# Performance work log

Hardware: AMD Instinct MI355X
Metric: run time of the kernel (lower is better)

## Reference

```python
import jax, jax.numpy as jnp
import numpy as np

N = 50000      # nodes
E = 800000     # edges
M = 1000000    # total subgraph membership rows
D = 128        # atom_fea_len
ED = 64        # nbr_fea_len
H = 8          # heads
C = D // H     # per-head dim


def _ln(x, g, b, eps=1e-5):
    mu = x.mean(-1, keepdims=True)
    var = ((x - mu) ** 2).mean(-1, keepdims=True)
    return (x - mu) / jnp.sqrt(var + eps) * g + b


def setup_inputs() -> dict:
    key = jax.random.key(0)
    ks = jax.random.split(key, 16)
    s = 0.05
    inp = {
        "x": jax.random.normal(ks[0], (N, D), jnp.float32),
        "edge_index": jax.random.randint(ks[1], (2, E), 0, N, jnp.int32),
        "edge_attr": jax.random.normal(ks[2], (E, ED), jnp.float32),
        "sub_nodes": jax.random.randint(ks[3], (M,), 0, N, jnp.int32),
        "sub_indicator": jax.random.randint(ks[4], (M,), 0, N, jnp.int32),
        # TransformerConv params (PyG: lin_query/key/value, lin_edge, lin_skip, all with bias)
        "Wq": jax.random.normal(ks[5], (D, D), jnp.float32) * s,
        "bq": jnp.zeros((D,), jnp.float32),
        "Wk": jax.random.normal(ks[6], (D, D), jnp.float32) * s,
        "bk": jnp.zeros((D,), jnp.float32),
        "Wv": jax.random.normal(ks[7], (D, D), jnp.float32) * s,
        "bv": jnp.zeros((D,), jnp.float32),
        "We": jax.random.normal(ks[8], (ED, D), jnp.float32) * s,
        "be": jnp.zeros((D,), jnp.float32),
        "Ws": jax.random.normal(ks[9], (D, D), jnp.float32) * s,
        "bs": jnp.zeros((D,), jnp.float32),
        # subgraph_norm
        "sn_g": jnp.ones((D,), jnp.float32),
        "sn_b": jnp.zeros((D,), jnp.float32),
        # subgraph_proj: Linear -> SiLU -> Linear
        "p1_w": jax.random.normal(ks[10], (D, D), jnp.float32) * s,
        "p1_b": jnp.zeros((D,), jnp.float32),
        "p2_w": jax.random.normal(ks[11], (D, D), jnp.float32) * s,
        "p2_b": jnp.zeros((D,), jnp.float32),
        # out_norm
        "on_g": jnp.ones((D,), jnp.float32),
        "on_b": jnp.zeros((D,), jnp.float32),
    }
    return inp


def reference(x, edge_index, edge_attr, sub_nodes, sub_indicator,
              Wq, bq, Wk, bk, Wv, bv, We, be, Ws, bs,
              sn_g, sn_b, p1_w, p1_b, p2_w, p2_b, on_g, on_b):
    n = x.shape[0]
    src, dst = edge_index[0], edge_index[1]  # messages flow src -> dst (PyG source_to_target)

    # ---- TransformerConv ----
    q = (x @ Wq + bq).reshape(n, H, C)
    k = (x @ Wk + bk).reshape(n, H, C)
    v = (x @ Wv + bv).reshape(n, H, C)
    e = (edge_attr @ We + be).reshape(-1, H, C)       # [E,H,C]
    ke = k[src] + e                                    # edge-conditioned keys
    ve = v[src] + e                                    # edge-conditioned values
    alpha = (q[dst] * ke).sum(-1) / jnp.sqrt(jnp.asarray(C, x.dtype))  # [E,H]
    # scatter-softmax over incoming edges of each dst node
    m = jax.ops.segment_max(alpha, dst, num_segments=n)               # [N,H]
    ea = jnp.exp(alpha - m[dst])
    denom = jax.ops.segment_sum(ea, dst, num_segments=n)              # [N,H]
    num = jax.ops.segment_sum(ea[:, :, None] * ve, dst, num_segments=n)  # [N,H,C]
    attn = num / jnp.where(denom > 0, denom, 1.0)[:, :, None]
    x_trans = attn.reshape(n, H * C) + (x @ Ws + bs)   # concat heads + root skip

    # ---- subgraph branch: gather -> LayerNorm -> MLP -> scatter-mean ----
    sx = x[sub_nodes]                                  # [M,D]
    sx = _ln(sx, sn_g, sn_b)
    sx = jax.nn.silu(sx @ p1_w + p1_b) @ p2_w + p2_b
    cnt = jax.ops.segment_sum(jnp.ones((sx.shape[0],), x.dtype), sub_indicator, num_segments=n)
    sub_x = jax.ops.segment_sum(sx, sub_indicator, num_segments=n) / jnp.maximum(cnt, 1.0)[:, None]

    # ---- combine (dropout is identity in eval) ----
    out = _ln(x + x_trans + sub_x, on_g, on_b)
    return jax.nn.silu(out)
```

## Files before the change

### kernel.cpp

```cpp
#include <hip/hip_runtime.h>
#include <math.h>

#define DD 128
#define EDD 64

typedef __attribute__((ext_vector_type(8))) short bf16x8;
typedef __attribute__((ext_vector_type(4))) float f32x4;

__device__ inline unsigned short f2bf(float f) {
    unsigned int u = __float_as_uint(f);
    u += 0x7FFFu + ((u >> 16) & 1u);
    return (unsigned short)(u >> 16);
}
__device__ inline unsigned int pack2bf16(float lo, float hi) {
    return (unsigned int)f2bf(lo) | ((unsigned int)f2bf(hi) << 16);
}
__device__ inline float bflo(unsigned int u) { return __uint_as_float(u << 16); }
__device__ inline float bfhi(unsigned int u) { return __uint_as_float(u & 0xffff0000u); }

__global__ __launch_bounds__(256) void packw6_kernel(
    const float* __restrict__ w0, const float* __restrict__ w1, const float* __restrict__ w2,
    const float* __restrict__ w3, const float* __restrict__ w4, const float* __restrict__ w5,
    unsigned short* __restrict__ packed)
{
    int which = blockIdx.y;
    const float* w = which == 0 ? w0 : which == 1 ? w1 : which == 2 ? w2
                   : which == 3 ? w3 : which == 4 ? w4 : w5;
    unsigned short* pk = packed + (size_t)which * DD * DD;
    int idx = blockIdx.x * 256 + threadIdx.x;
    if (idx >= DD * DD) return;
    int j    = idx & 7;
    int lane = (idx >> 3) & 63;
    int kt   = (idx >> 9) & 3;
    int ncf  = idx >> 11;
    int kk  = kt * 32 + (lane >> 4) * 8 + j;
    int col = ncf * 16 + (lane & 15);
    pk[idx] = f2bf(w[kk * DD + col]);
}

__device__ inline void gemm_b(const bf16x8 af[4][2], const unsigned short* __restrict__ packB,
                              int wc, int lane, f32x4 acc[2][4])
{
    #pragma unroll
    for (int i = 0; i < 2; i++)
        #pragma unroll
        for (int j = 0; j < 4; j++) acc[i][j] = (f32x4){0.f, 0.f, 0.f, 0.f};
    #pragma unroll
    for (int kt = 0; kt < 4; kt++) {
        #pragma unroll
        for (int nc = 0; nc < 4; nc++) {
            bf16x8 b = *(const bf16x8*)&packB[(((wc * 4 + nc) * 4 + kt) * 64 + lane) * 8];
            acc[0][nc] = __builtin_amdgcn_mfma_f32_16x16x32_bf16(af[kt][0], b, acc[0][nc], 0, 0, 0);
            acc[1][nc] = __builtin_amdgcn_mfma_f32_16x16x32_bf16(af[kt][1], b, acc[1][nc], 0, 0, 0);
        }
    }
}

__global__ __launch_bounds__(256, 4) void lin4_mfma_kernel(
    const float* __restrict__ x,
    const unsigned short* __restrict__ packBq, const float* __restrict__ bq,
    const unsigned short* __restrict__ packBk, const float* __restrict__ bk,
    const unsigned short* __restrict__ packBv, const float* __restrict__ bv,
    const unsigned short* __restrict__ packBs, const float* __restrict__ bs,
    const float* __restrict__ sn_g, const float* __restrict__ sn_b,
    float* __restrict__ q, unsigned short* __restrict__ kplane, unsigned short* __restrict__ vplane,
    float* __restrict__ pre, unsigned int* __restrict__ lnx, int N)
{
    __shared__ unsigned short sxs[64 * DD];
    int tid = threadIdx.x;
    int lane = tid & 63, wid = tid >> 6;
    size_t m0 = (size_t)blockIdx.x * 64;

    {
        float g0 = sn_g[2 * lane], g1 = sn_g[2 * lane + 1];
        float b0 = sn_b[2 * lane], b1 = sn_b[2 * lane + 1];
        #pragma unroll
        for (int r = 0; r < 16; r++) {
            int tr = wid * 16 + r;
            size_t row = m0 + tr;
            float v0 = 0.f, v1 = 0.f;
            if (row < (size_t)N) {
                float2 xv = *(const float2*)&x[row * DD + 2 * lane];
                v0 = xv.x; v1 = xv.y;
            }
            unsigned int uidx = ((unsigned)(tr * 64 + lane)) ^ (((unsigned)tr & 7u) << 2);
            ((unsigned int*)sxs)[uidx] = pack2bf16(v0, v1);
            float s1 = v0 + v1, s2 = v0 * v0 + v1 * v1;
            #pragma unroll
            for (int o = 32; o >= 1; o >>= 1) { s1 += __shfl_xor(s1, o); s2 += __shfl_xor(s2, o); }
            float mean = s1 * (1.f / DD);
            float var  = s2 * (1.f / DD) - mean * mean;
            float rs = rsqrtf(var + 1e-5f);
            if (row < (size_t)N)
                lnx[row * 64 + lane] = pack2bf16((v0 - mean) * rs * g0 + b0,
                                                 (v1 - mean) * rs * g1 + b1);
        }
    }
    __syncthreads();

    int wr = wid >> 1, wc = wid & 1;
    int rA = wr * 32 + (lane & 15);
    int kb = (lane >> 4) * 8;

    bf16x8 af[4][2];
    #pragma unroll
    for (int kt = 0; kt < 4; kt++) {
        int k0 = kt * 32 + kb;
        af[kt][0] = *(const bf16x8*)&sxs[((rA)      * DD + k0) ^ ((rA & 7) << 3)];
        int rA1 = rA + 16;
        af[kt][1] = *(const bf16x8*)&sxs[((rA1)     * DD + k0) ^ ((rA1 & 7) << 3)];
    }

    f32x4 acc[2][4];
    int colb = wc * 64 + (lane & 15);
    int jrow = (lane >> 4) * 4;

    gemm_b(af, packBq, wc, lane, acc);
    #pragma unroll
    for (int mrf = 0; mrf < 2; mrf++) {
        int rbase = wr * 32 + mrf * 16 + jrow;
        #pragma unroll
        for (int nc = 0; nc < 4; nc++) {
            int col = colb + nc * 16;
            float bias = bq[col];
            #pragma unroll
            for (int j = 0; j < 4; j++) {
                size_t row = m0 + rbase + j;
                if (row < (size_t)N) q[row * DD + col] = acc[mrf][nc][j] + bias;
            }
        }
    }
    gemm_b(af, packBk, wc, lane, acc);
    #pragma unroll
    for (int mrf = 0; mrf < 2; mrf++) {
        int rbase = wr * 32 + mrf * 16 + jrow;
        #pragma unroll
        for (int nc = 0; nc < 4; nc++) {
            int col = colb + nc * 16;
            float bias = bk[col];
            #pragma unroll
            for (int j = 0; j < 4; j++) {
                size_t row = m0 + rbase + j;
                if (row < (size_t)N) kplane[row * DD + col] = f2bf(acc[mrf][nc][j] + bias);
            }
        }
    }
    gemm_b(af, packBv, wc, lane, acc);
    #pragma unroll
    for (int mrf = 0; mrf < 2; mrf++) {
        int rbase = wr * 32 + mrf * 16 + jrow;
        #pragma unroll
        for (int nc = 0; nc < 4; nc++) {
            int col = colb + nc * 16;
            float bias = bv[col];
            #pragma unroll
            for (int j = 0; j < 4; j++) {
                size_t row = m0 + rbase + j;
                if (row < (size_t)N) vplane[row * DD + col] = f2bf(acc[mrf][nc][j] + bias);
            }
        }
    }
    gemm_b(af, packBs, wc, lane, acc);
    #pragma unroll
    for (int mrf = 0; mrf < 2; mrf++) {
        int rbase = wr * 32 + mrf * 16 + jrow;
        #pragma unroll
        for (int nc = 0; nc < 4; nc++) {
            int col = colb + nc * 16;
            float bias = bs[col];
            #pragma unroll
            for (int j = 0; j < 4; j++) {
                size_t row = m0 + rbase + j;
                if (row < (size_t)N)
                    pre[row * DD + col] = x[row * DD + col] + acc[mrf][nc][j] + bias;
            }
        }
    }
}

__global__ __launch_bounds__(256, 4) void mlpnode_kernel(
    const unsigned int* __restrict__ lnx,
    const unsigned short* __restrict__ packB1, const float* __restrict__ p1b,
    const unsigned short* __restrict__ packB2, const float* __restrict__ p2b,
    unsigned short* __restrict__ fnode, int N)
{
    __shared__ unsigned short sxs[64 * DD];
    int tid = threadIdx.x;
    int lane = tid & 63, wid = tid >> 6;
    size_t m0 = (size_t)blockIdx.x * 64;

    #pragma unroll
    for (int r = 0; r < 16; r++) {
        int tr = wid * 16 + r;
        size_t row = m0 + tr;
        unsigned int val = (row < (size_t)N) ? lnx[row * 64 + lane] : 0u;
        unsigned int uidx = ((unsigned)(tr * 64 + lane)) ^ (((unsigned)tr & 7u) << 2);
        ((unsigned int*)sxs)[uidx] = val;
    }
    __syncthreads();

    int wr = wid >> 1, wc = wid & 1;
    int rA = wr * 32 + (lane & 15);
    int kb = (lane >> 4) * 8;

    f32x4 acc[2][4];
    #pragma unroll
    for (int i = 0; i < 2; i++)
        #pragma unroll
        for (int j = 0; j < 4; j++) acc[i][j] = (f32x4){0.f, 0.f, 0.f, 0.f};
    #pragma unroll
    for (int kt = 0; kt < 4; kt++) {
        int k0 = kt * 32 + kb;
        bf16x8 a0 = *(const bf16x8*)&sxs[((rA)  * DD + k0) ^ ((rA & 7) << 3)];
        int rA1 = rA + 16;
        bf16x8 a1 = *(const bf16x8*)&sxs[((rA1) * DD + k0) ^ ((rA1 & 7) << 3)];
        #pragma unroll
        for (int nc = 0; nc < 4; nc++) {
            bf16x8 b = *(const bf16x8*)&packB1[(((wc * 4 + nc) * 4 + kt) * 64 + lane) * 8];
            acc[0][nc] = __builtin_amdgcn_mfma_f32_16x16x32_bf16(a0, b, acc[0][nc], 0, 0, 0);
            acc[1][nc] = __builtin_amdgcn_mfma_f32_16x16x32_bf16(a1, b, acc[1][nc], 0, 0, 0);
        }
    }
    __syncthreads();

    {
        float bias1[4];
        #pragma unroll
        for (int nc = 0; nc < 4; nc++) bias1[nc] = p1b[wc * 64 + nc * 16 + (lane & 15)];
        #pragma unroll
        for (int mrf = 0; mrf < 2; mrf++) {
            int rbase = wr * 32 + mrf * 16 + (lane >> 4) * 4;
            #pragma unroll
            for (int nc = 0; nc < 4; nc++) {
                int col = wc * 64 + nc * 16 + (lane & 15);
                #pragma unroll
                for (int j = 0; j < 4; j++) {
                    float h = acc[mrf][nc][j] + bias1[nc];
                    h = h / (1.f + __expf(-h));
                    int rr = rbase + j;
                    sxs[(rr * DD + col) ^ ((rr & 7) << 3)] = f2bf(h);
                }
            }
        }
    }
    __syncthreads();

    f32x4 acc2[2][4];
    #pragma unroll
    for (int i = 0; i < 2; i++)
        #pragma unroll
        for (int j = 0; j < 4; j++) acc2[i][j] = (f32x4){0.f, 0.f, 0.f, 0.f};
    #pragma unroll
    for (int kt = 0; kt < 4; kt++) {
        int k0 = kt * 32 + kb;
        bf16x8 a0 = *(const bf16x8*)&sxs[((rA)  * DD + k0) ^ ((rA & 7) << 3)];
        int rA1 = rA + 16;
        bf16x8 a1 = *(const bf16x8*)&sxs[((rA1) * DD + k0) ^ ((rA1 & 7) << 3)];
        #pragma unroll
        for (int nc = 0; nc < 4; nc++) {
            bf16x8 b = *(const bf16x8*)&packB2[(((wc * 4 + nc) * 4 + kt) * 64 + lane) * 8];
            acc2[0][nc] = __builtin_amdgcn_mfma_f32_16x16x32_bf16(a0, b, acc2[0][nc], 0, 0, 0);
            acc2[1][nc] = __builtin_amdgcn_mfma_f32_16x16x32_bf16(a1, b, acc2[1][nc], 0, 0, 0);
        }
    }

    {
        float bias2[4];
        #pragma unroll
        for (int nc = 0; nc < 4; nc++) bias2[nc] = p2b[wc * 64 + nc * 16 + (lane & 15)];
        #pragma unroll
        for (int mrf = 0; mrf < 2; mrf++) {
            int rbase = wr * 32 + mrf * 16 + (lane >> 4) * 4;
            #pragma unroll
            for (int nc = 0; nc < 4; nc++) {
                int col = wc * 64 + nc * 16 + (lane & 15);
                #pragma unroll
                for (int j = 0; j < 4; j++) {
                    size_t row = m0 + rbase + j;
                    if (row < (size_t)N)
                        fnode[row * DD + col] = f2bf(acc2[mrf][nc][j] + bias2[nc]);
                }
            }
        }
    }
}

__global__ void count2_kernel(const int* __restrict__ dstA, int E,
                              const int* __restrict__ sub_ind, int M,
                              int* __restrict__ deg, int* __restrict__ cnt)
{
    int i = blockIdx.x * blockDim.x + threadIdx.x;
    int stride = gridDim.x * blockDim.x;
    int total = E > M ? E : M;
    for (; i < total; i += stride) {
        if (i < E) atomicAdd(&deg[dstA[i]], 1);
        if (i < M) atomicAdd(&cnt[sub_ind[i]], 1);
    }
}

__global__ __launch_bounds__(1024) void bscan_kernel(
    const int* __restrict__ inA, const int* __restrict__ inB,
    int* __restrict__ exA, int* __restrict__ exB,
    int* __restrict__ bsA, int* __restrict__ bsB, int N)
{
    const int* in = blockIdx.y ? inB : inA;
    int* ex = blockIdx.y ? exB : exA;
    int* bs = blockIdx.y ? bsB : bsA;
    __shared__ int s[1024];
    int tid = threadIdx.x;
    int i = blockIdx.x * 1024 + tid;
    int val = (i < N) ? in[i] : 0;
    s[tid] = val; __syncthreads();
    for (int off = 1; off < 1024; off <<= 1) {
        int t = (tid >= off) ? s[tid - off] : 0;
        __syncthreads();
        s[tid] += t;
        __syncthreads();
    }
    if (i < N) ex[i] = s[tid] - val;
    if (tid == 1023) bs[blockIdx.x] = s[1023];
}

__global__ void bsum_kernel(int* __restrict__ bsA, int* __restrict__ bsB,
                            int* __restrict__ indptrA, int* __restrict__ indptrB,
                            int nb, int N)
{
    int which = threadIdx.x;
    if (which < 2) {
        int* bs = which ? bsB : bsA;
        int* indptr = which ? indptrB : indptrA;
        int run = 0;
        for (int b = 0; b < nb; b++) { int v = bs[b]; bs[b] = run; run += v; }
        indptr[N] = run;
    }
}

__global__ void bfix_kernel(int* __restrict__ exA, int* __restrict__ fillA, const int* __restrict__ bsA,
                            int* __restrict__ exB, int* __restrict__ fillB, const int* __restrict__ bsB,
                            int N)
{
    int i = blockIdx.x * blockDim.x + threadIdx.x;
    if (i < N) {
        int vA = exA[i] + bsA[i >> 10];
        exA[i] = vA; fillA[i] = vA;
        int vB = exB[i] + bsB[i >> 10];
        exB[i] = vB; fillB[i] = vB;
    }
}

__global__ void escatter_kernel(const int* __restrict__ srcA, const int* __restrict__ dstA, int E,
                                int* __restrict__ fill, int2* __restrict__ spair)
{
    int i = blockIdx.x * blockDim.x + threadIdx.x;
    int stride = gridDim.x * blockDim.x;
    for (; i < E; i += stride) {
        int d = dstA[i];
        int pos = atomicAdd(&fill[d], 1);
        spair[pos] = make_int2(srcA[i], i);
    }
}

__global__ void sscatter_kernel(const int* __restrict__ sub_nodes, const int* __restrict__ sub_ind,
                                int M, int* __restrict__ sfill, int* __restrict__ snode)
{
    int i = blockIdx.x * blockDim.x + threadIdx.x;
    int stride = gridDim.x * blockDim.x;
    for (; i < M; i += stride) {
        int seg = sub_ind[i];
        int pos = atomicAdd(&sfill[seg], 1);
        snode[pos] = sub_nodes[i];
    }
}

__global__ __launch_bounds__(256) void qprep_kernel(
    const float* __restrict__ q, const float* __restrict__ We,
    unsigned int* __restrict__ qweU, int N)
{
    int tid = threadIdx.x;
    int wave = tid >> 6, lane = tid & 63;
    int n = blockIdx.x * 4 + wave;
    if (n >= N) return;
    int jj = lane & 7, g = lane >> 3;
    int hc0 = g * 16;
    const float4* qp = (const float4*)&q[(size_t)n * DD + hc0];
    float4 q0 = qp[0], q1 = qp[1], q2 = qp[2], q3 = qp[3];
    float qWe[8];
    #pragma unroll
    for (int r = 0; r < 8; r++) {
        const float4* wp = (const float4*)&We[(size_t)(8 * jj + r) * DD + hc0];
        float4 wa = wp[0], wb = wp[1], wc = wp[2], wd = wp[3];
        qWe[r] = q0.x * wa.x + q0.y * wa.y + q0.z * wa.z + q0.w * wa.w
               + q1.x * wb.x + q1.y * wb.y + q1.z * wb.z + q1.w * wb.w
               + q2.x * wc.x + q2.y * wc.y + q2.z * wc.z + q2.w * wc.w
               + q3.x * wd.x + q3.y * wd.y + q3.z * wd.z + q3.w * wd.w;
    }
    uint4 packed;
    packed.x = pack2bf16(qWe[0], qWe[1]);
    packed.y = pack2bf16(qWe[2], qWe[3]);
    packed.z = pack2bf16(qWe[4], qWe[5]);
    packed.w = pack2bf16(qWe[6], qWe[7]);
    *(uint4*)&qweU[(size_t)n * 256 + 4 * lane] = packed;
}

__global__ __launch_bounds__(256, 5) void attn_kernel(
    const float* __restrict__ q,
    const unsigned int* __restrict__ kplane32, const unsigned int* __restrict__ vplane32,
    const float* __restrict__ edge_attr, const unsigned int* __restrict__ qweU,
    const float* __restrict__ We, const float* __restrict__ be,
    const int* __restrict__ indptr, const int2* __restrict__ spair,
    float* __restrict__ pre, int N)
{
    int tid = threadIdx.x;
    int wave = tid >> 6, lane = tid & 63;
    int n = blockIdx.x * 4 + wave;
    if (n >= N) return;

    int gbase = lane & 56;
    int jj = lane & 7;
    int c0 = lane * 2;

    float2 qv  = *(const float2*)&q[(size_t)n * DD + c0];
    float2 bev = *(const float2*)&be[c0];

    float t = qv.x * bev.x + qv.y * bev.y;
    t += __shfl_xor(t, 1); t += __shfl_xor(t, 2); t += __shfl_xor(t, 4);
    float qbe4 = t * 0.25f;

    uint4 qw = *(const uint4*)&qweU[(size_t)n * 256 + 4 * lane];
    float qwe0 = bflo(qw.x), qwe1 = bfhi(qw.x), qwe2 = bflo(qw.y), qwe3 = bfhi(qw.y);
    float qwe4 = bflo(qw.z), qwe5 = bfhi(qw.z), qwe6 = bflo(qw.w), qwe7 = bfhi(qw.w);

    int start = indptr[n], end = indptr[n + 1];
    float s = 0.f, av0 = 0.f, av1 = 0.f;
    float aea[8];
    #pragma unroll
    for (int r = 0; r < 8; r++) aea[r] = 0.f;

    int ii = start;
    for (; ii + 3 < end; ii += 4) {
        int2 se[4];
        #pragma unroll
        for (int u = 0; u < 4; u++) se[u] = spair[ii + u];
        float4 ea0[4], ea1[4];
        unsigned int ku[4], vu[4];
        #pragma unroll
        for (int u = 0; u < 4; u++) {
            const float4* eap = (const float4*)&edge_attr[(size_t)se[u].y * EDD + 8 * jj];
            ea0[u] = eap[0];
            ea1[u] = eap[1];
            ku[u] = kplane32[(size_t)se[u].x * 64 + lane];
            vu[u] = vplane32[(size_t)se[u].x * 64 + lane];
        }
        float p[4];
        #pragma unroll
        for (int u = 0; u < 4; u++) {
            float part = qv.x * bflo(ku[u]) + qv.y * bfhi(ku[u])
                       + ea0[u].x * qwe0 + ea0[u].y * qwe1 + ea0[u].z * qwe2 + ea0[u].w * qwe3
                       + ea1[u].x * qwe4 + ea1[u].y * qwe5 + ea1[u].z * qwe6 + ea1[u].w * qwe7;
            part += __shfl_xor(part, 1);
            part += __shfl_xor(part, 2);
            part += __shfl_xor(part, 4);
            p[u] = __expf(part * 0.25f + qbe4);
        }
        #pragma unroll
        for (int u = 0; u < 4; u++) {
            s += p[u];
            av0 += p[u] * bflo(vu[u]);
            av1 += p[u] * bfhi(vu[u]);
            aea[0] += p[u] * ea0[u].x; aea[1] += p[u] * ea0[u].y;
            aea[2] += p[u] * ea0[u].z; aea[3] += p[u] * ea0[u].w;
            aea[4] += p[u] * ea1[u].x; aea[5] += p[u] * ea1[u].y;
            aea[6] += p[u] * ea1[u].z; aea[7] += p[u] * ea1[u].w;
        }
    }
    for (; ii < end; ii++) {
        int2 se = spair[ii];
        const float4* eap = (const float4*)&edge_attr[(size_t)se.y * EDD + 8 * jj];
        float4 ea0 = eap[0];
        float4 ea1 = eap[1];
        unsigned int ku = kplane32[(size_t)se.x * 64 + lane];
        unsigned int vu = vplane32[(size_t)se.x * 64 + lane];
        float part = qv.x * bflo(ku) + qv.y * bfhi(ku)
                   + ea0.x * qwe0 + ea0.y * qwe1 + ea0.z * qwe2 + ea0.w * qwe3
                   + ea1.x * qwe4 + ea1.y * qwe5 + ea1.z * qwe6 + ea1.w * qwe7;
        part += __shfl_xor(part, 1);
        part += __shfl_xor(part, 2);
        part += __shfl_xor(part, 4);
        float p = __expf(part * 0.25f + qbe4);
        s += p;
        av0 += p * bflo(vu);
        av1 += p * bfhi(vu);
        aea[0] += p * ea0.x; aea[1] += p * ea0.y; aea[2] += p * ea0.z; aea[3] += p * ea0.w;
        aea[4] += p * ea1.x; aea[5] += p * ea1.y; aea[6] += p * ea1.z; aea[7] += p * ea1.w;
    }

    if (end > start) {
        float inv = 1.f / s;
        float oe0 = 0.f, oe1 = 0.f;
        #pragma unroll
        for (int m = 0; m < 8; m++) {
            #pragma unroll
            for (int r = 0; r < 8; r++) {
                float a = __shfl(aea[r], gbase + m);
                float2 w = *(const float2*)&We[(size_t)(8 * m + r) * DD + c0];
                oe0 += a * w.x;
                oe1 += a * w.y;
            }
        }
        size_t o = (size_t)n * DD + c0;
        pre[o]     += (av0 + oe0) * inv + bev.x;
        pre[o + 1] += (av1 + oe1) * inv + bev.y;
    }
}

__global__ __launch_bounds__(256) void final2_kernel(
    const float* __restrict__ pre, const unsigned int* __restrict__ fnodeU,
    const int* __restrict__ sindptr, const int* __restrict__ snode,
    const float* __restrict__ on_g, const float* __restrict__ on_b,
    float* __restrict__ out, int N)
{
    int tid = threadIdx.x;
    int wave = tid >> 6, lane = tid & 63;
    int n = blockIdx.x * 4 + wave;
    if (n >= N) return;
    int c0 = 2 * lane;

    int start = sindptr[n], end = sindptr[n + 1];
    float sum0 = 0.f, sum1 = 0.f;
    int ii = start;
    for (; ii + 3 < end; ii += 4) {
        int n0 = snode[ii], n1 = snode[ii + 1], n2 = snode[ii + 2], n3 = snode[ii + 3];
        unsigned int u0 = fnodeU[(size_t)n0 * 64 + lane];
        unsigned int u1 = fnodeU[(size_t)n1 * 64 + lane];
        unsigned int u2 = fnodeU[(size_t)n2 * 64 + lane];
        unsigned int u3 = fnodeU[(size_t)n3 * 64 + lane];
        sum0 += bflo(u0) + bflo(u1) + bflo(u2) + bflo(u3);
        sum1 += bfhi(u0) + bfhi(u1) + bfhi(u2) + bfhi(u3);
    }
    for (; ii < end; ii++) {
        unsigned int u = fnodeU[(size_t)snode[ii] * 64 + lane];
        sum0 += bflo(u);
        sum1 += bfhi(u);
    }
    float inv = 1.f / fmaxf((float)(end - start), 1.f);

    float2 pv = *(const float2*)&pre[(size_t)n * DD + c0];
    float v0 = pv.x + sum0 * inv;
    float v1 = pv.y + sum1 * inv;

    float s1 = v0 + v1, s2 = v0 * v0 + v1 * v1;
    #pragma unroll
    for (int off = 32; off >= 1; off >>= 1) { s1 += __shfl_xor(s1, off); s2 += __shfl_xor(s2, off); }
    float mean = s1 * (1.f / DD);
    float var  = s2 * (1.f / DD) - mean * mean;
    float rs = rsqrtf(var + 1e-5f);

    float2 gv = *(const float2*)&on_g[c0];
    float2 bv = *(const float2*)&on_b[c0];
    float ov0 = (v0 - mean) * rs * gv.x + bv.x;
    float ov1 = (v1 - mean) * rs * gv.y + bv.y;
    float2 res;
    res.x = ov0 / (1.f + __expf(-ov0));
    res.y = ov1 / (1.f + __expf(-ov1));
    *(float2*)&out[(size_t)n * DD + c0] = res;
}

extern "C" void kernel_launch(void* const* d_in, const int* in_sizes, int n_in,
                              void* d_out, int out_size, void* d_ws, size_t ws_size,
                              hipStream_t stream)
{
    const float* x         = (const float*)d_in[0];
    const int*   edge_index= (const int*)  d_in[1];
    const float* edge_attr = (const float*)d_in[2];
    const int*   sub_nodes = (const int*)  d_in[3];
    const int*   sub_ind   = (const int*)  d_in[4];
    const float* Wq = (const float*)d_in[5];  const float* bq = (const float*)d_in[6];
    const float* Wk = (const float*)d_in[7];  const float* bk = (const float*)d_in[8];
    const float* Wv = (const float*)d_in[9];  const float* bv = (const float*)d_in[10];
    const float* We = (const float*)d_in[11]; const float* be = (const float*)d_in[12];
    const float* Ws = (const float*)d_in[13]; const float* bs = (const float*)d_in[14];
    const float* sn_g = (const float*)d_in[15]; const float* sn_b = (const float*)d_in[16];
    const float* p1w = (const float*)d_in[17]; const float* p1b = (const float*)d_in[18];
    const float* p2w = (const float*)d_in[19]; const float* p2b = (const float*)d_in[20];
    const float* on_g = (const float*)d_in[21]; const float* on_b = (const float*)d_in[22];

    int N = in_sizes[0] / DD;
    int E = in_sizes[1] / 2;
    int M = in_sizes[3];
    float* out = (float*)d_out;

    unsigned short* packAll = (unsigned short*)d_ws;
    unsigned short* packB1 = packAll;
    unsigned short* packB2 = packB1 + DD * DD;
    unsigned short* packBq = packB2 + DD * DD;
    unsigned short* packBk = packBq + DD * DD;
    unsigned short* packBv = packBk + DD * DD;
    unsigned short* packBs = packBv + DD * DD;
    size_t ND = (size_t)N * DD;
    float* q     = (float*)(packBs + DD * DD);
    unsigned short* kplane = (unsigned short*)(q + ND);
    unsigned short* vplane = kplane + ND;
    float* pre   = (float*)(vplane + ND);
    unsigned int* qweU  = (unsigned int*)(pre + ND);
    unsigned int* lnx   = qweU + (size_t)N * 256;
    unsigned int* fnode = lnx + (size_t)N * 64;
    int2* spair  = (int2*)(fnode + (size_t)N * 64);
    int* indptr  = (int*)(spair + E);
    int* fill    = indptr + (N + 1);
    int* deg     = fill + N;
    int* cnt     = deg + N;
    int* sindptr = cnt + N;
    int* sfill   = sindptr + (N + 1);
    int* snode   = sfill + N;
    int* bsA     = snode + M;
    int* bsB     = bsA + 64;

    const int* srcA = edge_index;
    const int* dstA = edge_index + E;

    int nb = (N + 1023) / 1024;

    hipMemsetAsync(deg, 0, (size_t)2 * N * sizeof(int), stream);

    {
        dim3 g(64, 6);
        packw6_kernel<<<g, 256, 0, stream>>>(p1w, p2w, Wq, Wk, Wv, Ws, packAll);
    }

    lin4_mfma_kernel<<<(N + 63) / 64, 256, 0, stream>>>(x, packBq, bq, packBk, bk, packBv, bv,
                                                        packBs, bs, sn_g, sn_b,
                                                        q, kplane, vplane, pre, lnx, N);
    mlpnode_kernel<<<(N + 63) / 64, 256, 0, stream>>>(lnx, packB1, p1b, packB2, p2b,
                                                      (unsigned short*)fnode, N);
    count2_kernel<<<2048, 256, 0, stream>>>(dstA, E, sub_ind, M, deg, cnt);
    {
        dim3 g(nb, 2);
        bscan_kernel<<<g, 1024, 0, stream>>>(deg, cnt, indptr, sindptr, bsA, bsB, N);
    }
    bsum_kernel<<<1, 64, 0, stream>>>(bsA, bsB, indptr, sindptr, nb, N);
    bfix_kernel<<<(N + 255) / 256, 256, 0, stream>>>(indptr, fill, bsA, sindptr, sfill, bsB, N);
    escatter_kernel<<<2048, 256, 0, stream>>>(srcA, dstA, E, fill, spair);
    sscatter_kernel<<<2048, 256, 0, stream>>>(sub_nodes, sub_ind, M, sfill, snode);
    qprep_kernel<<<(N + 3) / 4, 256, 0, stream>>>(q, We, qweU, N);
    attn_kernel<<<(N + 3) / 4, 256, 0, stream>>>(q, (const unsigned int*)kplane,
                                                 (const unsigned int*)vplane, edge_attr, qweU,
                                                 We, be, indptr, spair, pre, N);
    final2_kernel<<<(N + 3) / 4, 256, 0, stream>>>(pre, fnode, sindptr, snode, on_g, on_b, out, N);
}
```

Before: 736.6 us.

## Store q in bf16, fuse edge and subgraph scatters, unroll attention by six

```diff
diff --git a/kernel.cpp b/kernel.cpp
--- a/kernel.cpp
+++ b/kernel.cpp
@@ -63,7 +63,8 @@
     const unsigned short* __restrict__ packBv, const float* __restrict__ bv,
     const unsigned short* __restrict__ packBs, const float* __restrict__ bs,
     const float* __restrict__ sn_g, const float* __restrict__ sn_b,
-    float* __restrict__ q, unsigned short* __restrict__ kplane, unsigned short* __restrict__ vplane,
+    unsigned short* __restrict__ qplane,
+    unsigned short* __restrict__ kplane, unsigned short* __restrict__ vplane,
     float* __restrict__ pre, unsigned int* __restrict__ lnx, int N)
 {
     __shared__ unsigned short sxs[64 * DD];
@@ -126,7 +127,7 @@
             #pragma unroll
             for (int j = 0; j < 4; j++) {
                 size_t row = m0 + rbase + j;
-                if (row < (size_t)N) q[row * DD + col] = acc[mrf][nc][j] + bias;
+                if (row < (size_t)N) qplane[row * DD + col] = f2bf(acc[mrf][nc][j] + bias);
             }
         }
     }
@@ -348,32 +349,30 @@
     }
 }
 
-__global__ void escatter_kernel(const int* __restrict__ srcA, const int* __restrict__ dstA, int E,
-                                int* __restrict__ fill, int2* __restrict__ spair)
+__global__ void scatter2_kernel(const int* __restrict__ srcA, const int* __restrict__ dstA, int E,
+                                int* __restrict__ fill, int2* __restrict__ spair,
+                                const int* __restrict__ sub_nodes, const int* __restrict__ sub_ind,
+                                int M, int* __restrict__ sfill, int* __restrict__ snode)
 {
     int i = blockIdx.x * blockDim.x + threadIdx.x;
     int stride = gridDim.x * blockDim.x;
-    for (; i < E; i += stride) {
-        int d = dstA[i];
-        int pos = atomicAdd(&fill[d], 1);
-        spair[pos] = make_int2(srcA[i], i);
-    }
-}
-
-__global__ void sscatter_kernel(const int* __restrict__ sub_nodes, const int* __restrict__ sub_ind,
-                                int M, int* __restrict__ sfill, int* __restrict__ snode)
-{
-    int i = blockIdx.x * blockDim.x + threadIdx.x;
-    int stride = gridDim.x * blockDim.x;
-    for (; i < M; i += stride) {
-        int seg = sub_ind[i];
-        int pos = atomicAdd(&sfill[seg], 1);
-        snode[pos] = sub_nodes[i];
+    int total = E > M ? E : M;
+    for (; i < total; i += stride) {
+        if (i < E) {
+            int d = dstA[i];
+            int pos = atomicAdd(&fill[d], 1);
+            spair[pos] = make_int2(srcA[i], i);
+        }
+        if (i < M) {
+            int seg = sub_ind[i];
+            int pos = atomicAdd(&sfill[seg], 1);
+            snode[pos] = sub_nodes[i];
+        }
     }
 }
 
 __global__ __launch_bounds__(256) void qprep_kernel(
-    const float* __restrict__ q, const float* __restrict__ We,
+    const unsigned int* __restrict__ qplane32, const float* __restrict__ We,
     unsigned int* __restrict__ qweU, int N)
 {
     int tid = threadIdx.x;
@@ -382,17 +381,22 @@
     if (n >= N) return;
     int jj = lane & 7, g = lane >> 3;
     int hc0 = g * 16;
-    const float4* qp = (const float4*)&q[(size_t)n * DD + hc0];
-    float4 q0 = qp[0], q1 = qp[1], q2 = qp[2], q3 = qp[3];
+    uint4 qa = *(const uint4*)&qplane32[(size_t)n * 64 + hc0 / 2];
+    uint4 qb = *(const uint4*)&qplane32[(size_t)n * 64 + hc0 / 2 + 4];
+    float qs[16];
+    qs[0] = bflo(qa.x); qs[1] = bfhi(qa.x); qs[2] = bflo(qa.y); qs[3] = bfhi(qa.y);
+    qs[4] = bflo(qa.z); qs[5] = bfhi(qa.z); qs[6] = bflo(qa.w); qs[7] = bfhi(qa.w);
+    qs[8] = bflo(qb.x); qs[9] = bfhi(qb.x); qs[10] = bflo(qb.y); qs[11] = bfhi(qb.y);
+    qs[12] = bflo(qb.z); qs[13] = bfhi(qb.z); qs[14] = bflo(qb.w); qs[15] = bfhi(qb.w);
     float qWe[8];
     #pragma unroll
     for (int r = 0; r < 8; r++) {
         const float4* wp = (const float4*)&We[(size_t)(8 * jj + r) * DD + hc0];
         float4 wa = wp[0], wb = wp[1], wc = wp[2], wd = wp[3];
-        qWe[r] = q0.x * wa.x + q0.y * wa.y + q0.z * wa.z + q0.w * wa.w
-               + q1.x * wb.x + q1.y * wb.y + q1.z * wb.z + q1.w * wb.w
-               + q2.x * wc.x + q2.y * wc.y + q2.z * wc.z + q2.w * wc.w
-               + q3.x * wd.x + q3.y * wd.y + q3.z * wd.z + q3.w * wd.w;
+        qWe[r] = qs[0]  * wa.x + qs[1]  * wa.y + qs[2]  * wa.z + qs[3]  * wa.w
+               + qs[4]  * wb.x + qs[5]  * wb.y + qs[6]  * wb.z + qs[7]  * wb.w
+               + qs[8]  * wc.x + qs[9]  * wc.y + qs[10] * wc.z + qs[11] * wc.w
+               + qs[12] * wd.x + qs[13] * wd.y + qs[14] * wd.z + qs[15] * wd.w;
     }
     uint4 packed;
     packed.x = pack2bf16(qWe[0], qWe[1]);
@@ -402,8 +406,8 @@
     *(uint4*)&qweU[(size_t)n * 256 + 4 * lane] = packed;
 }
 
-__global__ __launch_bounds__(256, 5) void attn_kernel(
-    const float* __restrict__ q,
+__global__ __launch_bounds__(256, 4) void attn_kernel(
+    const unsigned int* __restrict__ qplane32,
     const unsigned int* __restrict__ kplane32, const unsigned int* __restrict__ vplane32,
     const float* __restrict__ edge_attr, const unsigned int* __restrict__ qweU,
     const float* __restrict__ We, const float* __restrict__ be,
@@ -419,10 +423,11 @@
     int jj = lane & 7;
     int c0 = lane * 2;
 
-    float2 qv  = *(const float2*)&q[(size_t)n * DD + c0];
+    unsigned int qu = qplane32[(size_t)n * 64 + lane];
+    float qvx = bflo(qu), qvy = bfhi(qu);
     float2 bev = *(const float2*)&be[c0];
 
-    float t = qv.x * bev.x + qv.y * bev.y;
+    float t = qvx * bev.x + qvy * bev.y;
     t += __shfl_xor(t, 1); t += __shfl_xor(t, 2); t += __shfl_xor(t, 4);
     float qbe4 = t * 0.25f;
 
@@ -437,24 +442,24 @@
     for (int r = 0; r < 8; r++) aea[r] = 0.f;
 
     int ii = start;
-    for (; ii + 3 < end; ii += 4) {
-        int2 se[4];
-        #pragma unroll
-        for (int u = 0; u < 4; u++) se[u] = spair[ii + u];
-        float4 ea0[4], ea1[4];
-        unsigned int ku[4], vu[4];
-        #pragma unroll
-        for (int u = 0; u < 4; u++) {
+    for (; ii + 5 < end; ii += 6) {
+        int2 se[6];
+        #pragma unroll
+        for (int u = 0; u < 6; u++) se[u] = spair[ii + u];
+        float4 ea0[6], ea1[6];
+        unsigned int ku[6], vu[6];
+        #pragma unroll
+        for (int u = 0; u < 6; u++) {
             const float4* eap = (const float4*)&edge_attr[(size_t)se[u].y * EDD + 8 * jj];
             ea0[u] = eap[0];
             ea1[u] = eap[1];
             ku[u] = kplane32[(size_t)se[u].x * 64 + lane];
             vu[u] = vplane32[(size_t)se[u].x * 64 + lane];
         }
-        float p[4];
-        #pragma unroll
-        for (int u = 0; u < 4; u++) {
-            float part = qv.x * bflo(ku[u]) + qv.y * bfhi(ku[u])
+        float p[6];
+        #pragma unroll
+        for (int u = 0; u < 6; u++) {
+            float part = qvx * bflo(ku[u]) + qvy * bfhi(ku[u])
                        + ea0[u].x * qwe0 + ea0[u].y * qwe1 + ea0[u].z * qwe2 + ea0[u].w * qwe3
                        + ea1[u].x * qwe4 + ea1[u].y * qwe5 + ea1[u].z * qwe6 + ea1[u].w * qwe7;
             part += __shfl_xor(part, 1);
@@ -463,7 +468,7 @@
             p[u] = __expf(part * 0.25f + qbe4);
         }
         #pragma unroll
-        for (int u = 0; u < 4; u++) {
+        for (int u = 0; u < 6; u++) {
             s += p[u];
             av0 += p[u] * bflo(vu[u]);
             av1 += p[u] * bfhi(vu[u]);
@@ -480,7 +485,7 @@
         float4 ea1 = eap[1];
         unsigned int ku = kplane32[(size_t)se.x * 64 + lane];
         unsigned int vu = vplane32[(size_t)se.x * 64 + lane];
-        float part = qv.x * bflo(ku) + qv.y * bfhi(ku)
+        float part = qvx * bflo(ku) + qvy * bfhi(ku)
                    + ea0.x * qwe0 + ea0.y * qwe1 + ea0.z * qwe2 + ea0.w * qwe3
                    + ea1.x * qwe4 + ea1.y * qwe5 + ea1.z * qwe6 + ea1.w * qwe7;
         part += __shfl_xor(part, 1);
@@ -597,8 +602,8 @@
     unsigned short* packBv = packBk + DD * DD;
     unsigned short* packBs = packBv + DD * DD;
     size_t ND = (size_t)N * DD;
-    float* q     = (float*)(packBs + DD * DD);
-    unsigned short* kplane = (unsigned short*)(q + ND);
+    unsigned short* qplane = (unsigned short*)(packBs + DD * DD);
+    unsigned short* kplane = qplane + ND;
     unsigned short* vplane = kplane + ND;
     float* pre   = (float*)(vplane + ND);
     unsigned int* qweU  = (unsigned int*)(pre + ND);
@@ -629,7 +634,7 @@
 
     lin4_mfma_kernel<<<(N + 63) / 64, 256, 0, stream>>>(x, packBq, bq, packBk, bk, packBv, bv,
                                                         packBs, bs, sn_g, sn_b,
-                                                        q, kplane, vplane, pre, lnx, N);
+                                                        qplane, kplane, vplane, pre, lnx, N);
     mlpnode_kernel<<<(N + 63) / 64, 256, 0, stream>>>(lnx, packB1, p1b, packB2, p2b,
                                                       (unsigned short*)fnode, N);
     count2_kernel<<<2048, 256, 0, stream>>>(dstA, E, sub_ind, M, deg, cnt);
@@ -639,10 +644,11 @@
     }
     bsum_kernel<<<1, 64, 0, stream>>>(bsA, bsB, indptr, sindptr, nb, N);
     bfix_kernel<<<(N + 255) / 256, 256, 0, stream>>>(indptr, fill, bsA, sindptr, sfill, bsB, N);
-    escatter_kernel<<<2048, 256, 0, stream>>>(srcA, dstA, E, fill, spair);
-    sscatter_kernel<<<2048, 256, 0, stream>>>(sub_nodes, sub_ind, M, sfill, snode);
-    qprep_kernel<<<(N + 3) / 4, 256, 0, stream>>>(q, We, qweU, N);
-    attn_kernel<<<(N + 3) / 4, 256, 0, stream>>>(q, (const unsigned int*)kplane,
+    scatter2_kernel<<<2048, 256, 0, stream>>>(srcA, dstA, E, fill, spair,
+                                              sub_nodes, sub_ind, M, sfill, snode);
+    qprep_kernel<<<(N + 3) / 4, 256, 0, stream>>>((const unsigned int*)qplane, We, qweU, N);
+    attn_kernel<<<(N + 3) / 4, 256, 0, stream>>>((const unsigned int*)qplane,
+                                                 (const unsigned int*)kplane,
                                                  (const unsigned int*)vplane, edge_attr, qweU,
                                                  We, be, indptr, spair, pre, N);
     final2_kernel<<<(N + 3) / 4, 256, 0, stream>>>(pre, fnode, sindptr, snode, on_g, on_b, out, N);
```

New measurement: 746.9 us. About the same (+1.4%).
